# Kernel optimization log

Hardware: AMD Instinct MI355X
Metric: run time of the kernel (lower is better)

Reference implementation:

```python
import jax, jax.numpy as jnp
import numpy as np

DEGREE = 8
HIDDEN = 256
IN_DIM = 3
N_LAYERS = 8  # num_hidden_layers=8 -> 1 input + 6 middle + 1 output ChebyKAN layers


def cheby_layer(x, coeff):
    """x: [P, in], coeff: [in, out, degree+1] -> [P, out].
    Computes tanh(x), Chebyshev recurrence T_0..T_d, and contracts
    sum_d T_d(x)_i * coeff[i, o, d] without materializing the full basis.
    """
    x = jnp.tanh(x)
    t_prev = jnp.ones_like(x)          # T_0
    t_cur = x                          # T_1
    out = jnp.einsum('pi,io->po', t_prev, coeff[:, :, 0])
    out = out + jnp.einsum('pi,io->po', t_cur, coeff[:, :, 1])
    for d in range(2, coeff.shape[-1]):
        t_prev, t_cur = t_cur, 2.0 * x * t_cur - t_prev
        out = out + jnp.einsum('pi,io->po', t_cur, coeff[:, :, d])
    return out


def decode(pts, ws):
    h = pts
    for w in ws:
        h = cheby_layer(h, w)
    return h


def setup_inputs() -> dict:
    key = jax.random.key(0)
    k_nm, k_m, *k_ws = jax.random.split(key, 2 + N_LAYERS)
    B, N = 4, 16384
    inp = {
        'non_mnfld_pnts': jax.random.normal(k_nm, (B, N, IN_DIM), dtype=jnp.float32),
        'mnfld_pnts': jax.random.normal(k_m, (B, N, IN_DIM), dtype=jnp.float32),
    }
    dims = [IN_DIM] + [HIDDEN] * (N_LAYERS - 1) + [1]
    for i in range(N_LAYERS):
        fan_in, fan_out = dims[i], dims[i + 1]
        std = 1.0 / (fan_in * (DEGREE + 1))
        inp[f'w{i}'] = jax.random.normal(k_ws[i], (fan_in, fan_out, DEGREE + 1), dtype=jnp.float32) * std
    return inp


def reference(non_mnfld_pnts, mnfld_pnts, w0, w1, w2, w3, w4, w5, w6, w7):
    ws = [w0, w1, w2, w3, w4, w5, w6, w7]
    B = non_mnfld_pnts.shape[0]
    mnfld_pred = decode(mnfld_pnts.reshape(-1, IN_DIM), ws).reshape(B, -1)
    nonmnfld_pred = decode(non_mnfld_pnts.reshape(-1, IN_DIM), ws).reshape(B, -1)
    return (mnfld_pred, nonmnfld_pred)
```

## Files before the change

kernel.cpp:

```cpp
#include <hip/hip_runtime.h>

typedef _Float16 f16;
typedef __attribute__((ext_vector_type(4)))  _Float16 f16x4;
typedef __attribute__((ext_vector_type(8)))  _Float16 f16x8;
typedef __attribute__((ext_vector_type(16))) float    f32x16;

#define WT_L (8*256*256)

__device__ __forceinline__ float fexp2(float x) {
#if __has_builtin(__builtin_amdgcn_exp2f)
    return __builtin_amdgcn_exp2f(x);
#else
    return exp2f(x);
#endif
}

__device__ __forceinline__ float fast_tanh(float v) {
    float a = __builtin_fabsf(v);
    float e = fexp2(a * -2.8853900817779268f);
    float r = (1.0f - e) * __builtin_amdgcn_rcpf(1.0f + e);
    return __builtin_copysignf(r, v);
}

__global__ void prep_mid(const float* __restrict__ w, f16* __restrict__ wt, float* __restrict__ biasL) {
    __shared__ float red[256];
    const int i = threadIdx.x;
    const int o = blockIdx.x;
    float v[9];
#pragma unroll
    for (int d = 0; d < 9; d++) v[d] = w[(i*256 + o)*9 + d];
#pragma unroll
    for (int d = 1; d < 9; d++) wt[((d-1)*256 + o)*256 + i] = (f16)v[d];
    red[i] = v[0];
    __syncthreads();
#pragma unroll
    for (int s = 128; s > 0; s >>= 1) {
        if (i < s) red[i] += red[i + s];
        __syncthreads();
    }
    if (i == 0) biasL[o] = red[0];
}

__global__ void prep_w0(const float* __restrict__ w0, float* __restrict__ w0t) {
    int id = blockIdx.x*256 + threadIdx.x;
    int i = id / 2304, rem = id % 2304;
    int o = rem / 9, d = rem % 9;
    w0t[(i*9 + d)*256 + o] = w0[id];
}

__global__ void prep_w7(const float* __restrict__ w7, float* __restrict__ w7p) {
    int id = blockIdx.x*256 + threadIdx.x;
    int ch = id / 9, d = id % 9;
    w7p[ch*12 + d] = w7[id];
}

__global__ void k0(const float* __restrict__ nonm, const float* __restrict__ mnf,
                   const float* __restrict__ w0t, f16* __restrict__ xg) {
    const int t = threadIdx.x, b = blockIdx.x;
    const int pt = t & 63;
    const int oh = (t >> 6) * 64;
    const int pid = b*64 + pt;
    const float* src = (pid < 65536) ? mnf : nonm;
    const int sp = (pid < 65536) ? pid : pid - 65536;
    float c0 = src[sp*3 + 0];
    float c1 = src[sp*3 + 1];
    float c2 = src[sp*3 + 2];
    float xx[3] = {fast_tanh(c0), fast_tanh(c1), fast_tanh(c2)};
    float bas[27];
#pragma unroll
    for (int i = 0; i < 3; i++) {
        float t0 = 1.0f, t1 = xx[i];
        bas[i*9+0] = t0; bas[i*9+1] = t1;
        float x2 = xx[i] + xx[i];
#pragma unroll
        for (int d = 2; d < 9; d++) {
            float t2 = x2*t1 - t0;
            bas[i*9+d] = t2; t0 = t1; t1 = t2;
        }
    }
#pragma unroll 1
    for (int q = 0; q < 16; q++) {
        int o = oh + q*4;
        float4 a = {0.f, 0.f, 0.f, 0.f};
#pragma unroll
        for (int k = 0; k < 27; k++) {
            float4 wv = *(const float4*)(w0t + k*256 + o);
            a.x = fmaf(bas[k], wv.x, a.x);
            a.y = fmaf(bas[k], wv.y, a.y);
            a.z = fmaf(bas[k], wv.z, a.z);
            a.w = fmaf(bas[k], wv.w, a.w);
        }
        f16x4 hv = {(f16)fast_tanh(a.x), (f16)fast_tanh(a.y),
                    (f16)fast_tanh(a.z), (f16)fast_tanh(a.w)};
        *(f16x4*)(xg + (size_t)pid*256 + o) = hv;
    }
}

__global__ __launch_bounds__(256, 2)
void k_mid(const f16* __restrict__ wl, const float* __restrict__ biasL,
           f16* __restrict__ xg)
{
    __shared__ __align__(16) f16 xs[128*256];

    const int t    = threadIdx.x;
    const int b    = blockIdx.x;
    const int lane = t & 63;
    const int w    = t >> 6;
    const int l31  = lane & 31;
    const int half = lane >> 5;
    const int nb   = w * 64;
    const size_t tile_off = (size_t)b * 128 * 256;

#pragma unroll
    for (int i = 0; i < 16; i++) {
        int idx = i*256 + t;
        int pt = idx >> 5, cu = idx & 31;
        f16x8 v = *(const f16x8*)(xg + tile_off + (size_t)idx*8);
        *(f16x8*)(xs + pt*256 + ((cu ^ (pt & 7))*8)) = v;
    }
    __syncthreads();

    f32x16 acc[4][2];
    const f16x8 ones = {(f16)1.f,(f16)1.f,(f16)1.f,(f16)1.f,(f16)1.f,(f16)1.f,(f16)1.f,(f16)1.f};

    const f16* wbase = wl + half*8 + (nb + l31)*256;
    float b0 = biasL[nb + l31];
    float b1 = biasL[nb + 32 + l31];
#pragma unroll
    for (int mt = 0; mt < 4; mt++)
#pragma unroll
        for (int r = 0; r < 16; r++) { acc[mt][0][r] = b0; acc[mt][1][r] = b1; }

    f16x8 xv[4], Bb[4][2];
#pragma unroll
    for (int mt = 0; mt < 4; mt++) {
        int m = mt*32 + l31;
        int unit = half ^ (m & 7);
        xv[mt] = *(const f16x8*)(xs + m*256 + unit*8);
    }
#pragma unroll
    for (int j = 0; j < 4; j++) {
        Bb[j][0] = *(const f16x8*)(wbase + j*65536);
        Bb[j][1] = *(const f16x8*)(wbase + j*65536 + 8192);
    }

    f16x8 x2[4], t1[4], t0[4];
#pragma unroll 1
    for (int ck = 0; ck < 16; ck++) {
        const int ckn = (ck < 15) ? ck + 1 : 15;
#pragma unroll
        for (int mt = 0; mt < 4; mt++) {
            t1[mt] = xv[mt];
            x2[mt] = xv[mt] + xv[mt];
            t0[mt] = ones;
        }
#pragma unroll
        for (int mt = 0; mt < 4; mt++) {
            int m = mt*32 + l31;
            int unit = (ckn*2 + half) ^ (m & 7);
            xv[mt] = *(const f16x8*)(xs + m*256 + unit*8);
        }
#pragma unroll
        for (int j = 0; j < 8; j++) {
            const int ck2 = (j < 4) ? ck : ckn;
            const int j2  = (j < 4) ? (j + 4) : (j - 4);
            f16x8 pb0 = *(const f16x8*)(wbase + ck2*16 + j2*65536);
            f16x8 pb1 = *(const f16x8*)(wbase + ck2*16 + j2*65536 + 8192);
#pragma unroll
            for (int mt = 0; mt < 4; mt++) {
                acc[mt][0] = __builtin_amdgcn_mfma_f32_32x32x16_f16(t1[mt], Bb[j&3][0], acc[mt][0], 0, 0, 0);
                acc[mt][1] = __builtin_amdgcn_mfma_f32_32x32x16_f16(t1[mt], Bb[j&3][1], acc[mt][1], 0, 0, 0);
            }
            if (j < 7) {
#pragma unroll
                for (int mt = 0; mt < 4; mt++) {
                    f16x8 tn = x2[mt]*t1[mt] - t0[mt];
                    t0[mt] = t1[mt];
                    t1[mt] = tn;
                }
            }
            Bb[j&3][0] = pb0;
            Bb[j&3][1] = pb1;
        }
    }
    __syncthreads();

#pragma unroll
    for (int mt = 0; mt < 4; mt++) {
#pragma unroll
        for (int nt = 0; nt < 2; nt++) {
            int ch = nb + nt*32 + l31;
            int cu = ch >> 3, ce = ch & 7;
#pragma unroll
            for (int r = 0; r < 16; r++) {
                int p = mt*32 + (r & 3) + 8*(r >> 2) + 4*half;
                int unit = cu ^ (p & 7);
                xs[p*256 + unit*8 + ce] = (f16)fast_tanh(acc[mt][nt][r]);
            }
        }
    }
    __syncthreads();

#pragma unroll
    for (int i = 0; i < 16; i++) {
        int idx = i*256 + t;
        int pt = idx >> 5, cu = idx & 31;
        f16x8 v = *(const f16x8*)(xs + pt*256 + ((cu ^ (pt & 7))*8));
        *(f16x8*)(xg + tile_off + (size_t)idx*8) = v;
    }
}

__global__ void k7(const f16* __restrict__ xg, const float* __restrict__ w7p,
                   float* __restrict__ out) {
    __shared__ float w7s[256*12];
    const int t = threadIdx.x, b = blockIdx.x;
#pragma unroll
    for (int i = 0; i < 12; i++) w7s[i*256 + t] = w7p[i*256 + t];
    __syncthreads();
    const int pid = b*256 + t;
    const f16* row = xg + (size_t)pid*256;
    float s = 0.0f;
#pragma unroll 1
    for (int cu = 0; cu < 32; cu++) {
        f16x8 xv = *(const f16x8*)(row + cu*8);
#pragma unroll
        for (int e = 0; e < 8; e++) {
            int ch = cu*8 + e;
            const float* wr = w7s + ch*12;
            float x = (float)xv[e];
            float x2 = x + x;
            float t0 = 1.0f, t1v = x;
            s = fmaf(wr[0], t0, s);
            s = fmaf(wr[1], t1v, s);
            float t2 = x2*t1v - t0;  s = fmaf(wr[2], t2, s);
            float t3 = x2*t2 - t1v;  s = fmaf(wr[3], t3, s);
            float t4 = x2*t3 - t2;   s = fmaf(wr[4], t4, s);
            float t5 = x2*t4 - t3;   s = fmaf(wr[5], t5, s);
            float t6 = x2*t5 - t4;   s = fmaf(wr[6], t6, s);
            float t7 = x2*t6 - t5;   s = fmaf(wr[7], t7, s);
            float t8 = x2*t7 - t6;   s = fmaf(wr[8], t8, s);
        }
    }
    out[pid] = s;
}

extern "C" void kernel_launch(void* const* d_in, const int* in_sizes, int n_in,
                              void* d_out, int out_size, void* d_ws, size_t ws_size,
                              hipStream_t stream) {
    const float* nonm = (const float*)d_in[0];
    const float* mnf  = (const float*)d_in[1];

    char* ws = (char*)d_ws;
    f16*   wtp   = (f16*)ws;
    float* biasp = (float*)(ws + 6*WT_L*2);
    float* w0tp  = (float*)(ws + 6*WT_L*2 + 6144);
    float* w7pp  = (float*)(ws + 6*WT_L*2 + 6144 + 27648);
    f16*   xg    = (f16*)(ws + 6*WT_L*2 + 6144 + 27648 + 12288);

    for (int L = 0; L < 6; L++)
        prep_mid<<<256, 256, 0, stream>>>((const float*)d_in[3 + L], wtp + L*WT_L, biasp + L*256);
    prep_w0<<<27, 256, 0, stream>>>((const float*)d_in[2], w0tp);
    prep_w7<<<9, 256, 0, stream>>>((const float*)d_in[9], w7pp);

    k0<<<2048, 256, 0, stream>>>(nonm, mnf, w0tp, xg);
    for (int L = 0; L < 6; L++)
        k_mid<<<1024, 256, 0, stream>>>(wtp + L*WT_L, biasp + L*256, xg);
    k7<<<512, 256, 0, stream>>>(xg, w7pp, (float*)d_out);
}
```

Baseline: 1.233 ms.

## Fuse weight prep kernels and pre-swizzle mid weights into MFMA lane order

Merges the six per-layer prep_mid launches plus prep_w0 and prep_w7 into one prep_all kernel, cutting launch overhead. Mid-layer weights are now stored in a layout matching the MFMA B-operand lane order (chunk, wave, n-tile, lane, element), so each wave's 16-byte loads in k_mid cover one contiguous block instead of rows strided by 256 halves. This aims to improve global/L2 load coalescing for weight fetches in the main GEMM loop. The prep kernel's writes become scattered, but that cost is small.

After: 1.003 ms. 18.7% less time.

```diff
diff --git a/kernel.cpp b/kernel.cpp
--- a/kernel.cpp
+++ b/kernel.cpp
@@ -22,36 +22,48 @@
     return __builtin_copysignf(r, v);
 }
 
-__global__ void prep_mid(const float* __restrict__ w, f16* __restrict__ wt, float* __restrict__ biasL) {
+__global__ void prep_all(const float* __restrict__ w0, const float* __restrict__ w1,
+                         const float* __restrict__ w2, const float* __restrict__ w3,
+                         const float* __restrict__ w4, const float* __restrict__ w5,
+                         const float* __restrict__ w6, const float* __restrict__ w7,
+                         f16* __restrict__ wt, float* __restrict__ biasp,
+                         float* __restrict__ w0t, float* __restrict__ w7p)
+{
     __shared__ float red[256];
-    const int i = threadIdx.x;
-    const int o = blockIdx.x;
-    float v[9];
-#pragma unroll
-    for (int d = 0; d < 9; d++) v[d] = w[(i*256 + o)*9 + d];
-#pragma unroll
-    for (int d = 1; d < 9; d++) wt[((d-1)*256 + o)*256 + i] = (f16)v[d];
-    red[i] = v[0];
-    __syncthreads();
-#pragma unroll
-    for (int s = 128; s > 0; s >>= 1) {
-        if (i < s) red[i] += red[i + s];
+    const int bi = blockIdx.x, t = threadIdx.x;
+    if (bi < 1536) {
+        const int L = bi >> 8, o = bi & 255, i = t;
+        const float* w;
+        switch (L) { case 0: w = w1; break; case 1: w = w2; break; case 2: w = w3; break;
+                     case 3: w = w4; break; case 4: w = w5; break; default: w = w6; }
+        float v[9];
+#pragma unroll
+        for (int d = 0; d < 9; d++) v[d] = w[(i*256 + o)*9 + d];
+        const int ck = i >> 4, k = i & 15;
+        const int wv4 = o >> 6, nt = (o >> 5) & 1, l31 = o & 31;
+        const int lane = (k >> 3)*32 + l31, e = k & 7;
+        const int base = ck*4096 + wv4*1024 + nt*512 + lane*8 + e;
+#pragma unroll
+        for (int d = 1; d < 9; d++)
+            wt[L*WT_L + (d-1)*16*4096 + base] = (f16)v[d];
+        red[i] = v[0];
         __syncthreads();
-    }
-    if (i == 0) biasL[o] = red[0];
-}
-
-__global__ void prep_w0(const float* __restrict__ w0, float* __restrict__ w0t) {
-    int id = blockIdx.x*256 + threadIdx.x;
-    int i = id / 2304, rem = id % 2304;
-    int o = rem / 9, d = rem % 9;
-    w0t[(i*9 + d)*256 + o] = w0[id];
-}
-
-__global__ void prep_w7(const float* __restrict__ w7, float* __restrict__ w7p) {
-    int id = blockIdx.x*256 + threadIdx.x;
-    int ch = id / 9, d = id % 9;
-    w7p[ch*12 + d] = w7[id];
+#pragma unroll
+        for (int s = 128; s > 0; s >>= 1) {
+            if (i < s) red[i] += red[i + s];
+            __syncthreads();
+        }
+        if (i == 0) biasp[L*256 + o] = red[0];
+    } else if (bi < 1563) {
+        int id = (bi - 1536)*256 + t;
+        int i = id / 2304, rem = id % 2304;
+        int o = rem / 9, d = rem % 9;
+        w0t[(i*9 + d)*256 + o] = w0[id];
+    } else {
+        int id = (bi - 1563)*256 + t;
+        int ch = id / 9, d = id % 9;
+        w7p[ch*12 + d] = w7[id];
+    }
 }
 
 __global__ void k0(const float* __restrict__ nonm, const float* __restrict__ mnf,
@@ -123,7 +135,7 @@
     f32x16 acc[4][2];
     const f16x8 ones = {(f16)1.f,(f16)1.f,(f16)1.f,(f16)1.f,(f16)1.f,(f16)1.f,(f16)1.f,(f16)1.f};
 
-    const f16* wbase = wl + half*8 + (nb + l31)*256;
+    const f16* wbase = wl + w*1024 + lane*8;
     float b0 = biasL[nb + l31];
     float b1 = biasL[nb + 32 + l31];
 #pragma unroll
@@ -140,8 +152,8 @@
     }
 #pragma unroll
     for (int j = 0; j < 4; j++) {
-        Bb[j][0] = *(const f16x8*)(wbase + j*65536);
-        Bb[j][1] = *(const f16x8*)(wbase + j*65536 + 8192);
+        Bb[j][0] = *(const f16x8*)(wbase + j*16*4096);
+        Bb[j][1] = *(const f16x8*)(wbase + j*16*4096 + 512);
     }
 
     f16x8 x2[4], t1[4], t0[4];
@@ -164,8 +176,9 @@
         for (int j = 0; j < 8; j++) {
             const int ck2 = (j < 4) ? ck : ckn;
             const int j2  = (j < 4) ? (j + 4) : (j - 4);
-            f16x8 pb0 = *(const f16x8*)(wbase + ck2*16 + j2*65536);
-            f16x8 pb1 = *(const f16x8*)(wbase + ck2*16 + j2*65536 + 8192);
+            const int off = (j2*16 + ck2)*4096;
+            f16x8 pb0 = *(const f16x8*)(wbase + off);
+            f16x8 pb1 = *(const f16x8*)(wbase + off + 512);
 #pragma unroll
             for (int mt = 0; mt < 4; mt++) {
                 acc[mt][0] = __builtin_amdgcn_mfma_f32_32x32x16_f16(t1[mt], Bb[j&3][0], acc[mt][0], 0, 0, 0);
@@ -257,10 +270,11 @@
     float* w7pp  = (float*)(ws + 6*WT_L*2 + 6144 + 27648);
     f16*   xg    = (f16*)(ws + 6*WT_L*2 + 6144 + 27648 + 12288);
 
-    for (int L = 0; L < 6; L++)
-        prep_mid<<<256, 256, 0, stream>>>((const float*)d_in[3 + L], wtp + L*WT_L, biasp + L*256);
-    prep_w0<<<27, 256, 0, stream>>>((const float*)d_in[2], w0tp);
-    prep_w7<<<9, 256, 0, stream>>>((const float*)d_in[9], w7pp);
+    prep_all<<<1572, 256, 0, stream>>>((const float*)d_in[2], (const float*)d_in[3],
+                                       (const float*)d_in[4], (const float*)d_in[5],
+                                       (const float*)d_in[6], (const float*)d_in[7],
+                                       (const float*)d_in[8], (const float*)d_in[9],
+                                       wtp, biasp, w0tp, w7pp);
 
     k0<<<2048, 256, 0, stream>>>(nonm, mnf, w0tp, xg);
     for (int L = 0; L < 6; L++)
```
